# Kernel tuning notes

Hardware: AMD Instinct MI355X
Metric: run time of the kernel (lower is better)

The kernel has to match this reference:

```python
import jax, jax.numpy as jnp
import numpy as np


def setup_inputs() -> dict:
    key = jax.random.key(0)
    k1, k2 = jax.random.split(key)
    n, c, h, w = 4, 64, 128, 128
    x = jax.random.normal(k1, (n, c, h, w), dtype=jnp.float32)
    # weight holds 9 stencil taps per channel, layout matches F.unfold: (n, c*9, h, w)
    weight = jax.random.normal(k2, (n, c * 9, h, w), dtype=jnp.float32)
    return {"x": x, "weight": weight, "max_step": 8}


def reference(x, weight, max_step):
    n, c, h, w = x.shape
    # normalize |w| over the 9 taps (done once, outside the loop, as in the original)
    wgt = jnp.abs(weight.reshape(n, c, 9, h, w))
    wgt = wgt / jnp.sum(wgt, axis=2, keepdims=True)

    steps = min(max_step, max(h, w))  # static Python ints -> static trip count

    def step(xx, _):
        # 3x3 patches via 9 shifted views of the padded image; tap order k = ki*3 + kj
        # matches F.unfold's row-major kernel ordering.
        xp = jnp.pad(xx, ((0, 0), (0, 0), (1, 1), (1, 1)))
        patches = jnp.stack(
            [xp[:, :, i:i + h, j:j + w] for i in range(3) for j in range(3)],
            axis=2,
        )  # (n, c, 9, h, w)
        return jnp.sum(patches * wgt, axis=2), None

    x_out, _ = jax.lax.scan(step, x, None, length=steps)
    return x_out
```

## Files before the change

kernel.cpp:

```cpp
#include <hip/hip_runtime.h>
#include <hip/hip_fp16.h>


constexpr int H = 128, W = 128, PLANE = H * W;
constexpr int NSTEP = 8;
constexpr int RPT  = 3;
constexpr int NRG  = 16;
constexpr int HALO = 8;
constexpr int OWN  = 32;

#define MKWIN(D, V) do {                                                     \
    (D)[1] = (V).x; (D)[2] = (V).y; (D)[3] = (V).z; (D)[4] = (V).w;          \
    float _l = __shfl_up((V).w, 1);                                          \
    float _r = __shfl_down((V).x, 1);                                        \
    (D)[0] = (quad == 0)  ? 0.f : _l;                                        \
    (D)[5] = (quad == 31) ? 0.f : _r;                                        \
} while (0)

__global__ __launch_bounds__(512)
void diff_fused(const float* __restrict__ xin,
                const float* __restrict__ wgt,
                float* __restrict__ out)
{
    __shared__ float ldsT[NRG][W];
    __shared__ float ldsB[NRG][W];

    const int tid   = threadIdx.x;
    const int quad  = tid & 31;
    const int rg    = tid >> 5;
    const int j0    = quad * 4;

    const int lb    = (blockIdx.x & 7) * 128 + (blockIdx.x >> 3);
    const int plane = lb >> 2;
    const int qtr   = lb & 3;
    const int rbase = qtr * OWN - HALO;
    const int r0    = rbase + rg * RPT;
    const size_t pbase = (size_t)plane * PLANE;

    const float* __restrict__ xp = xin + pbase;
    const float* __restrict__ wb = wgt + pbase * 9;

    float4 xr[RPT];
    #pragma unroll
    for (int p = 0; p < RPT; ++p) {
        const int gr = r0 + p;
        xr[p] = make_float4(0.f, 0.f, 0.f, 0.f);
        if ((unsigned)gr < (unsigned)H)
            xr[p] = *reinterpret_cast<const float4*>(xp + gr * W + j0);
    }

    __half2 wh[RPT][9][2];
    float s[RPT][4];
    #pragma unroll
    for (int p = 0; p < RPT; ++p) { s[p][0] = s[p][1] = s[p][2] = s[p][3] = 0.f; }

    #pragma unroll
    for (int k = 0; k < 9; ++k) {
        float4 v[RPT];
        #pragma unroll
        for (int p = 0; p < RPT; ++p) {
            const int gr = r0 + p;
            v[p] = make_float4(1.f, 1.f, 1.f, 1.f);
            if ((unsigned)gr < (unsigned)H)
                v[p] = *reinterpret_cast<const float4*>(
                           wb + (size_t)k * PLANE + gr * W + j0);
        }
        #pragma unroll
        for (int p = 0; p < RPT; ++p) {
            const float a0 = fabsf(v[p].x), a1 = fabsf(v[p].y);
            const float a2 = fabsf(v[p].z), a3 = fabsf(v[p].w);
            s[p][0] += a0; s[p][1] += a1; s[p][2] += a2; s[p][3] += a3;
            wh[p][k][0] = __halves2half2(__float2half_rn(a0), __float2half_rn(a1));
            wh[p][k][1] = __halves2half2(__float2half_rn(a2), __float2half_rn(a3));
        }
    }
    #pragma unroll
    for (int p = 0; p < RPT; ++p) {
        const float i0 = 1.f / s[p][0], i1 = 1.f / s[p][1];
        const float i2 = 1.f / s[p][2], i3 = 1.f / s[p][3];
        #pragma unroll
        for (int k = 0; k < 9; ++k) {
            wh[p][k][0] = __halves2half2(
                __float2half_rn(__low2float (wh[p][k][0]) * i0),
                __float2half_rn(__high2float(wh[p][k][0]) * i1));
            wh[p][k][1] = __halves2half2(
                __float2half_rn(__low2float (wh[p][k][1]) * i2),
                __float2half_rn(__high2float(wh[p][k][1]) * i3));
        }
    }

    #pragma unroll 1
    for (int st = 0; st < NSTEP; ++st) {
        *reinterpret_cast<float4*>(&ldsT[rg][j0]) = xr[0];
        *reinterpret_cast<float4*>(&ldsB[rg][j0]) = xr[RPT - 1];
        __syncthreads();
        float4 up = make_float4(0.f, 0.f, 0.f, 0.f);
        float4 dn = make_float4(0.f, 0.f, 0.f, 0.f);
        if (rg > 0)       up = *reinterpret_cast<const float4*>(&ldsB[rg - 1][j0]);
        if (rg < NRG - 1) dn = *reinterpret_cast<const float4*>(&ldsT[rg + 1][j0]);
        __syncthreads();

        float win[3][6];
        MKWIN(win[0], up);
        MKWIN(win[1], xr[0]);
        #pragma unroll
        for (int p = 0; p < RPT; ++p) {
            if (p < RPT - 1) { MKWIN(win[(p + 2) % 3], xr[p + 1]); }
            else             { MKWIN(win[(p + 2) % 3], dn); }
            float a0 = 0.f, a1 = 0.f, a2 = 0.f, a3 = 0.f;
            #pragma unroll
            for (int di = 0; di < 3; ++di) {
                #pragma unroll
                for (int dj = 0; dj < 3; ++dj) {
                    const int k = di * 3 + dj;
                    const __half2 w0 = wh[p][k][0];
                    const __half2 w1 = wh[p][k][1];
                    a0 = fmaf(__low2float (w0), win[(p + di) % 3][dj + 0], a0);
                    a1 = fmaf(__high2float(w0), win[(p + di) % 3][dj + 1], a1);
                    a2 = fmaf(__low2float (w1), win[(p + di) % 3][dj + 2], a2);
                    a3 = fmaf(__high2float(w1), win[(p + di) % 3][dj + 3], a3);
                }
            }
            xr[p] = make_float4(a0, a1, a2, a3);
        }
        #pragma unroll
        for (int p = 0; p < RPT; ++p) {
            const int gr = r0 + p;
            if ((unsigned)gr >= (unsigned)H)
                xr[p] = make_float4(0.f, 0.f, 0.f, 0.f);
        }
    }

    float* __restrict__ op = out + pbase;
    #pragma unroll
    for (int p = 0; p < RPT; ++p) {
        const int gr = r0 + p;
        const int lr = gr - rbase - HALO;
        if ((unsigned)lr < (unsigned)OWN)
            *reinterpret_cast<float4*>(op + gr * W + j0) = xr[p];
    }
}

extern "C" void kernel_launch(void* const* d_in, const int* in_sizes, int n_in,
                              void* d_out, int out_size, void* d_ws, size_t ws_size,
                              hipStream_t stream)
{
    const float* x = (const float*)d_in[0];
    const float* w = (const float*)d_in[1];
    float* out = (float*)d_out;
    (void)d_ws; (void)ws_size; (void)in_sizes; (void)n_in; (void)out_size;

    diff_fused<<<dim3(4 * 4 * 64), dim3(512), 0, stream>>>(x, w, out);
}
```

Baseline: 247.3 us.

## Enlarge row tile per block and spill last row's weights to LDS

Each block now owns half a plane (64 rows) with 5 rows per thread group instead of a quarter plane with 3 rows. This reduces the fraction of redundant halo rows whose weights and inputs are re-read. To limit register growth, the fifth row's normalized half-precision weights are stored in shared memory and read back each step. The grid halves, which lowers parallelism and adds LDS traffic in the inner loop.

```diff
diff --git a/kernel.cpp b/kernel.cpp
--- a/kernel.cpp
+++ b/kernel.cpp
@@ -4,10 +4,10 @@
 
 constexpr int H = 128, W = 128, PLANE = H * W;
 constexpr int NSTEP = 8;
-constexpr int RPT  = 3;
+constexpr int RPT  = 5;
 constexpr int NRG  = 16;
 constexpr int HALO = 8;
-constexpr int OWN  = 32;
+constexpr int OWN  = 64;
 
 #define MKWIN(D, V) do {                                                     \
     (D)[1] = (V).x; (D)[2] = (V).y; (D)[3] = (V).z; (D)[4] = (V).w;          \
@@ -24,32 +24,24 @@
 {
     __shared__ float ldsT[NRG][W];
     __shared__ float ldsB[NRG][W];
+    __shared__ uint2 whL[9][512];
 
     const int tid   = threadIdx.x;
     const int quad  = tid & 31;
     const int rg    = tid >> 5;
     const int j0    = quad * 4;
 
-    const int lb    = (blockIdx.x & 7) * 128 + (blockIdx.x >> 3);
-    const int plane = lb >> 2;
-    const int qtr   = lb & 3;
-    const int rbase = qtr * OWN - HALO;
+    const int lb    = (blockIdx.x & 7) * 64 + (blockIdx.x >> 3);
+    const int plane = lb >> 1;
+    const int half  = lb & 1;
+    const int rbase = half * OWN - HALO;
     const int r0    = rbase + rg * RPT;
     const size_t pbase = (size_t)plane * PLANE;
 
     const float* __restrict__ xp = xin + pbase;
     const float* __restrict__ wb = wgt + pbase * 9;
 
-    float4 xr[RPT];
-    #pragma unroll
-    for (int p = 0; p < RPT; ++p) {
-        const int gr = r0 + p;
-        xr[p] = make_float4(0.f, 0.f, 0.f, 0.f);
-        if ((unsigned)gr < (unsigned)H)
-            xr[p] = *reinterpret_cast<const float4*>(xp + gr * W + j0);
-    }
-
-    __half2 wh[RPT][9][2];
+    __half2 wh[RPT - 1][9][2];
     float s[RPT][4];
     #pragma unroll
     for (int p = 0; p < RPT; ++p) { s[p][0] = s[p][1] = s[p][2] = s[p][3] = 0.f; }
@@ -70,12 +62,19 @@
             const float a0 = fabsf(v[p].x), a1 = fabsf(v[p].y);
             const float a2 = fabsf(v[p].z), a3 = fabsf(v[p].w);
             s[p][0] += a0; s[p][1] += a1; s[p][2] += a2; s[p][3] += a3;
-            wh[p][k][0] = __halves2half2(__float2half_rn(a0), __float2half_rn(a1));
-            wh[p][k][1] = __halves2half2(__float2half_rn(a2), __float2half_rn(a3));
+            const __half2 h0 = __halves2half2(__float2half_rn(a0), __float2half_rn(a1));
+            const __half2 h1 = __halves2half2(__float2half_rn(a2), __float2half_rn(a3));
+            if (p < RPT - 1) {
+                wh[p][k][0] = h0;
+                wh[p][k][1] = h1;
+            } else {
+                whL[k][tid] = make_uint2(__builtin_bit_cast(unsigned int, h0),
+                                         __builtin_bit_cast(unsigned int, h1));
+            }
         }
     }
     #pragma unroll
-    for (int p = 0; p < RPT; ++p) {
+    for (int p = 0; p < RPT - 1; ++p) {
         const float i0 = 1.f / s[p][0], i1 = 1.f / s[p][1];
         const float i2 = 1.f / s[p][2], i3 = 1.f / s[p][3];
         #pragma unroll
@@ -87,6 +86,33 @@
                 __float2half_rn(__low2float (wh[p][k][1]) * i2),
                 __float2half_rn(__high2float(wh[p][k][1]) * i3));
         }
+    }
+    {
+        const float i0 = 1.f / s[RPT - 1][0], i1 = 1.f / s[RPT - 1][1];
+        const float i2 = 1.f / s[RPT - 1][2], i3 = 1.f / s[RPT - 1][3];
+        #pragma unroll
+        for (int k = 0; k < 9; ++k) {
+            const uint2 lv = whL[k][tid];
+            const __half2 h0 = __builtin_bit_cast(__half2, lv.x);
+            const __half2 h1 = __builtin_bit_cast(__half2, lv.y);
+            const __half2 n0 = __halves2half2(
+                __float2half_rn(__low2float (h0) * i0),
+                __float2half_rn(__high2float(h0) * i1));
+            const __half2 n1 = __halves2half2(
+                __float2half_rn(__low2float (h1) * i2),
+                __float2half_rn(__high2float(h1) * i3));
+            whL[k][tid] = make_uint2(__builtin_bit_cast(unsigned int, n0),
+                                     __builtin_bit_cast(unsigned int, n1));
+        }
+    }
+
+    float4 xr[RPT];
+    #pragma unroll
+    for (int p = 0; p < RPT; ++p) {
+        const int gr = r0 + p;
+        xr[p] = make_float4(0.f, 0.f, 0.f, 0.f);
+        if ((unsigned)gr < (unsigned)H)
+            xr[p] = *reinterpret_cast<const float4*>(xp + gr * W + j0);
     }
 
     #pragma unroll 1
@@ -113,8 +139,13 @@
                 #pragma unroll
                 for (int dj = 0; dj < 3; ++dj) {
                     const int k = di * 3 + dj;
-                    const __half2 w0 = wh[p][k][0];
-                    const __half2 w1 = wh[p][k][1];
+                    __half2 w0, w1;
+                    if (p < RPT - 1) { w0 = wh[p][k][0]; w1 = wh[p][k][1]; }
+                    else {
+                        const uint2 lv = whL[k][tid];
+                        w0 = __builtin_bit_cast(__half2, lv.x);
+                        w1 = __builtin_bit_cast(__half2, lv.y);
+                    }
                     a0 = fmaf(__low2float (w0), win[(p + di) % 3][dj + 0], a0);
                     a1 = fmaf(__high2float(w0), win[(p + di) % 3][dj + 1], a1);
                     a2 = fmaf(__low2float (w1), win[(p + di) % 3][dj + 2], a2);
@@ -135,7 +166,7 @@
     #pragma unroll
     for (int p = 0; p < RPT; ++p) {
         const int gr = r0 + p;
-        const int lr = gr - rbase - HALO;
+        const int lr = gr - half * OWN;
         if ((unsigned)lr < (unsigned)OWN)
             *reinterpret_cast<float4*>(op + gr * W + j0) = xr[p];
     }
@@ -150,5 +181,5 @@
     float* out = (float*)d_out;
     (void)d_ws; (void)ws_size; (void)in_sizes; (void)n_in; (void)out_size;
 
-    diff_fused<<<dim3(4 * 4 * 64), dim3(512), 0, stream>>>(x, w, out);
+    diff_fused<<<dim3(2 * 4 * 64), dim3(512), 0, stream>>>(x, w, out);
 }
```

Result: slower. 253.4 us (+2.5%).

## Skip halo rows outside dependency cone and exchange half of row boundaries via cross-half shuffles

Applied to the files above, without the earlier changes.

Each row's distance from the owned band is computed, and rows whose results cannot reach the owned output within the remaining steps skip their stencil FMAs. Rows too far from the band also skip loading their weights. The LDS boundary exchange is halved: neighbouring row groups in the same 64-wide wave swap rows with xor-32 shuffles, and only cross-wave neighbours go through a single shared array. The saving is less halo computation and weight traffic, at the cost of extra branches and a possible divergence penalty.

```diff
diff --git a/kernel.cpp b/kernel.cpp
--- a/kernel.cpp
+++ b/kernel.cpp
@@ -17,13 +17,21 @@
     (D)[5] = (quad == 31) ? 0.f : _r;                                        \
 } while (0)
 
+__device__ __forceinline__ float4 shflx32(float4 v) {
+    float4 r;
+    r.x = __shfl_xor(v.x, 32);
+    r.y = __shfl_xor(v.y, 32);
+    r.z = __shfl_xor(v.z, 32);
+    r.w = __shfl_xor(v.w, 32);
+    return r;
+}
+
 __global__ __launch_bounds__(512)
 void diff_fused(const float* __restrict__ xin,
                 const float* __restrict__ wgt,
                 float* __restrict__ out)
 {
-    __shared__ float ldsT[NRG][W];
-    __shared__ float ldsB[NRG][W];
+    __shared__ float ldsX[NRG][W];
 
     const int tid   = threadIdx.x;
     const int quad  = tid & 31;
@@ -35,18 +43,33 @@
     const int qtr   = lb & 3;
     const int rbase = qtr * OWN - HALO;
     const int r0    = rbase + rg * RPT;
+    const int own_lo = qtr * OWN;
+    const int own_hi = own_lo + OWN - 1;
     const size_t pbase = (size_t)plane * PLANE;
 
     const float* __restrict__ xp = xin + pbase;
     const float* __restrict__ wb = wgt + pbase * 9;
 
+    int  dist[RPT];
+    bool inr [RPT];
+    int  mind = 99;
+    #pragma unroll
+    for (int p = 0; p < RPT; ++p) {
+        const int gr = r0 + p;
+        inr[p] = (unsigned)gr < (unsigned)H;
+        int d = 0;
+        if (gr < own_lo)      d = own_lo - gr;
+        else if (gr > own_hi) d = gr - own_hi;
+        dist[p] = d;
+        if (inr[p] && d < mind) mind = d;
+    }
+
     float4 xr[RPT];
     #pragma unroll
     for (int p = 0; p < RPT; ++p) {
-        const int gr = r0 + p;
         xr[p] = make_float4(0.f, 0.f, 0.f, 0.f);
-        if ((unsigned)gr < (unsigned)H)
-            xr[p] = *reinterpret_cast<const float4*>(xp + gr * W + j0);
+        if (inr[p])
+            xr[p] = *reinterpret_cast<const float4*>(xp + (r0 + p) * W + j0);
     }
 
     __half2 wh[RPT][9][2];
@@ -59,11 +82,10 @@
         float4 v[RPT];
         #pragma unroll
         for (int p = 0; p < RPT; ++p) {
-            const int gr = r0 + p;
             v[p] = make_float4(1.f, 1.f, 1.f, 1.f);
-            if ((unsigned)gr < (unsigned)H)
+            if (inr[p] && dist[p] <= 7)
                 v[p] = *reinterpret_cast<const float4*>(
-                           wb + (size_t)k * PLANE + gr * W + j0);
+                           wb + (size_t)k * PLANE + (r0 + p) * W + j0);
         }
         #pragma unroll
         for (int p = 0; p < RPT; ++p) {
@@ -91,43 +113,51 @@
 
     #pragma unroll 1
     for (int st = 0; st < NSTEP; ++st) {
-        *reinterpret_cast<float4*>(&ldsT[rg][j0]) = xr[0];
-        *reinterpret_cast<float4*>(&ldsB[rg][j0]) = xr[RPT - 1];
+        *reinterpret_cast<float4*>(&ldsX[rg][j0]) =
+            (rg & 1) ? xr[RPT - 1] : xr[0];
         __syncthreads();
+
+        const float4 swT = shflx32(xr[0]);
+        const float4 swB = shflx32(xr[RPT - 1]);
         float4 up = make_float4(0.f, 0.f, 0.f, 0.f);
         float4 dn = make_float4(0.f, 0.f, 0.f, 0.f);
-        if (rg > 0)       up = *reinterpret_cast<const float4*>(&ldsB[rg - 1][j0]);
-        if (rg < NRG - 1) dn = *reinterpret_cast<const float4*>(&ldsT[rg + 1][j0]);
+        if (rg & 1) {
+            up = swB;
+            if (rg < NRG - 1)
+                dn = *reinterpret_cast<const float4*>(&ldsX[rg + 1][j0]);
+        } else {
+            dn = swT;
+            if (rg > 0)
+                up = *reinterpret_cast<const float4*>(&ldsX[rg - 1][j0]);
+        }
         __syncthreads();
 
-        float win[3][6];
-        MKWIN(win[0], up);
-        MKWIN(win[1], xr[0]);
-        #pragma unroll
-        for (int p = 0; p < RPT; ++p) {
-            if (p < RPT - 1) { MKWIN(win[(p + 2) % 3], xr[p + 1]); }
-            else             { MKWIN(win[(p + 2) % 3], dn); }
-            float a0 = 0.f, a1 = 0.f, a2 = 0.f, a3 = 0.f;
+        if (st + mind <= 7) {
+            float win[3][6];
+            MKWIN(win[0], up);
+            MKWIN(win[1], xr[0]);
             #pragma unroll
-            for (int di = 0; di < 3; ++di) {
-                #pragma unroll
-                for (int dj = 0; dj < 3; ++dj) {
-                    const int k = di * 3 + dj;
-                    const __half2 w0 = wh[p][k][0];
-                    const __half2 w1 = wh[p][k][1];
-                    a0 = fmaf(__low2float (w0), win[(p + di) % 3][dj + 0], a0);
-                    a1 = fmaf(__high2float(w0), win[(p + di) % 3][dj + 1], a1);
-                    a2 = fmaf(__low2float (w1), win[(p + di) % 3][dj + 2], a2);
-                    a3 = fmaf(__high2float(w1), win[(p + di) % 3][dj + 3], a3);
+            for (int p = 0; p < RPT; ++p) {
+                if (p < RPT - 1) { MKWIN(win[(p + 2) % 3], xr[p + 1]); }
+                else             { MKWIN(win[(p + 2) % 3], dn); }
+                if (inr[p] && st + dist[p] <= 7) {
+                    float a0 = 0.f, a1 = 0.f, a2 = 0.f, a3 = 0.f;
+                    #pragma unroll
+                    for (int di = 0; di < 3; ++di) {
+                        #pragma unroll
+                        for (int dj = 0; dj < 3; ++dj) {
+                            const int k = di * 3 + dj;
+                            const __half2 w0 = wh[p][k][0];
+                            const __half2 w1 = wh[p][k][1];
+                            a0 = fmaf(__low2float (w0), win[(p + di) % 3][dj + 0], a0);
+                            a1 = fmaf(__high2float(w0), win[(p + di) % 3][dj + 1], a1);
+                            a2 = fmaf(__low2float (w1), win[(p + di) % 3][dj + 2], a2);
+                            a3 = fmaf(__high2float(w1), win[(p + di) % 3][dj + 3], a3);
+                        }
+                    }
+                    xr[p] = make_float4(a0, a1, a2, a3);
                 }
             }
-            xr[p] = make_float4(a0, a1, a2, a3);
-        }
-        #pragma unroll
-        for (int p = 0; p < RPT; ++p) {
-            const int gr = r0 + p;
-            if ((unsigned)gr >= (unsigned)H)
-                xr[p] = make_float4(0.f, 0.f, 0.f, 0.f);
         }
     }
 
@@ -135,7 +165,7 @@
     #pragma unroll
     for (int p = 0; p < RPT; ++p) {
         const int gr = r0 + p;
-        const int lr = gr - rbase - HALO;
+        const int lr = gr - own_lo;
         if ((unsigned)lr < (unsigned)OWN)
             *reinterpret_cast<float4*>(op + gr * W + j0) = xr[p];
     }
```

New measurement: 262.6 us. +6.2%, slower.
